# Kernel tuning notes

Hardware: AMD Instinct MI355X
Metric: run time of the kernel (lower is better)

## Reference

```python
import jax, jax.numpy as jnp
import numpy as np

H = 512
B = 64
S = 2048
NUM_LAYERS = 1


def setup_inputs() -> dict:
    key = jax.random.key(0)
    ks = jax.random.split(key, 8)
    scale = 1.0 / np.sqrt(H)
    return {
        "hidden": jax.random.normal(ks[0], (NUM_LAYERS, B, H), dtype=jnp.float32),
        "encoder_outputs": jax.random.normal(ks[1], (B, S, H), dtype=jnp.float32),
        "U_w": jax.random.uniform(ks[2], (H, H), jnp.float32, -scale, scale),
        "U_b": jax.random.uniform(ks[3], (H,), jnp.float32, -scale, scale),
        "W_w": jax.random.uniform(ks[4], (H, H), jnp.float32, -scale, scale),
        "W_b": jax.random.uniform(ks[5], (H,), jnp.float32, -scale, scale),
        "V_w": jax.random.uniform(ks[6], (1, H), jnp.float32, -scale, scale),
        "V_b": jax.random.uniform(ks[7], (1,), jnp.float32, -scale, scale),
    }


def reference(hidden, encoder_outputs, U_w, U_b, W_w, W_b, V_w, V_b):
    # hidden: [L, B, H] -> take last layer, like hidden[-1]
    h = hidden[-1]  # [B, H]
    # Uatt(h): [B, H] -> broadcast over src_len
    u = h @ U_w.T + U_b            # [B, H]
    w = jnp.einsum('bsh,kh->bsk', encoder_outputs, W_w) + W_b  # [B, S, H]
    combined = jnp.tanh(u[:, None, :] + w)                     # [B, S, H]
    energy = jnp.einsum('bsh,h->bs', combined, V_w[0]) + V_b[0]  # [B, S]
    attn = jax.nn.softmax(energy, axis=1)                       # [B, S]
    context = jnp.einsum('bs,bsh->bh', attn, encoder_outputs)   # [B, H]
    return (context, attn)
```

## Files before the change

### kernel.cpp

```cpp
#include <hip/hip_runtime.h>
#include <hip/hip_bf16.h>

#define H 512
#define B 64
#define S 2048

typedef __bf16 bf16x8 __attribute__((ext_vector_type(8)));
typedef float f32x4 __attribute__((ext_vector_type(4)));
typedef unsigned int u32x4 __attribute__((ext_vector_type(4)));

__device__ __forceinline__ unsigned cvt2(float x, float y) {
    union { __hip_bfloat162 h; unsigned u; } cv;
    cv.h = __float22bfloat162_rn(make_float2(x, y));
    return cv.u;
}

__device__ __forceinline__ float fast_tanh(float x) {
    float e = __expf(2.0f * x);
    float r = __builtin_amdgcn_rcpf(e + 1.0f);
    return 1.0f - 2.0f * r;
}

__device__ __forceinline__ void gload_lds16(const void* g, void* l) {
    __builtin_amdgcn_global_load_lds(
        (const __attribute__((address_space(1))) unsigned int*)g,
        (__attribute__((address_space(3))) unsigned int*)l, 16, 0, 0);
}

__global__ __launch_bounds__(256) void w16_kernel(const float* __restrict__ Ww,
                                                  unsigned short* __restrict__ w16) {
    const int i = (blockIdx.x * 256 + threadIdx.x) * 8;
    float4 a = *(const float4*)(Ww + i);
    float4 b = *(const float4*)(Ww + i + 4);
    uint4 p;
    p.x = cvt2(a.x, a.y); p.y = cvt2(a.z, a.w);
    p.z = cvt2(b.x, b.y); p.w = cvt2(b.z, b.w);
    *(uint4*)(w16 + i) = p;
}

__global__ __launch_bounds__(256) void u_kernel(
        const float* __restrict__ hid, const float* __restrict__ Uw,
        const float* __restrict__ Ub, const float* __restrict__ Wb,
        float* __restrict__ u) {
    const int b = blockIdx.y;
    const int k = blockIdx.x * 4 + (threadIdx.x >> 6);
    const int lane = threadIdx.x & 63;
    const float4* wrow = (const float4*)(Uw + (size_t)k * H);
    const float4* hrow = (const float4*)(hid + (size_t)b * H);
    float4 w0 = wrow[lane * 2], w1 = wrow[lane * 2 + 1];
    float4 h0 = hrow[lane * 2], h1 = hrow[lane * 2 + 1];
    float acc = w0.x * h0.x + w0.y * h0.y + w0.z * h0.z + w0.w * h0.w
              + w1.x * h1.x + w1.y * h1.y + w1.z * h1.z + w1.w * h1.w;
    #pragma unroll
    for (int off = 1; off < 64; off <<= 1) acc += __shfl_xor(acc, off, 64);
    if (lane == 0) u[b * H + k] = acc + Ub[k] + Wb[k];
}

#define CN  32
#define NCH 16
#define CHB (CN * H * 2)

__global__ __launch_bounds__(512, 4) void energy_kernel(
        const float* __restrict__ enc, const unsigned short* __restrict__ w16,
        const float* __restrict__ Vw, const float* __restrict__ u,
        float* __restrict__ energy) {
    const int s0  = blockIdx.x * 128;
    const int b   = blockIdx.y;
    const int tid = threadIdx.x;
    const int wave = tid >> 6, lane = tid & 63;
    const int quad = lane >> 4, c = lane & 15;

    __shared__ unsigned char Bs[2][CHB];
    __shared__ float uS[H], vS[H];

    #pragma unroll
    for (int i = 0; i < 4; ++i) {
        const int row = i * 8 + wave;
        const int d   = (row << 10) + lane * 16;
        gload_lds16((const unsigned char*)w16 + (d ^ ((row & 7) << 4)),
                    &Bs[0][row << 10]);
    }

    uS[tid] = u[b * H + tid];
    vS[tid] = Vw[tid];

    u32x4 apack[16];
    {
        const float* pa = enc + ((size_t)(b * S + s0 + wave * 16 + c)) * H + quad * 8;
        #pragma unroll
        for (int half = 0; half < 2; ++half) {
            float4 x0[8], x1[8];
            #pragma unroll
            for (int q = 0; q < 8; ++q) {
                const int t = half * 8 + q;
                x0[q] = *(const float4*)(pa + t * 32);
                x1[q] = *(const float4*)(pa + t * 32 + 4);
            }
            #pragma unroll
            for (int q = 0; q < 8; ++q) {
                u32x4 p;
                p[0] = cvt2(x0[q].x, x0[q].y); p[1] = cvt2(x0[q].z, x0[q].w);
                p[2] = cvt2(x1[q].x, x1[q].y); p[3] = cvt2(x1[q].z, x1[q].w);
                apack[half * 8 + q] = p;
                asm volatile("" : "+v"(apack[half * 8 + q]));
            }
        }
    }

    float esum[4] = {};
    const int mask = (c & 7) << 4;

    #pragma unroll 2
    for (int cc = 0; cc < NCH; ++cc) {
        const int buf = cc & 1;
        if (cc) __syncthreads();
        if (cc < NCH - 1) {
            const unsigned char* src = (const unsigned char*)w16 + (cc + 1) * CHB;
            #pragma unroll
            for (int i = 0; i < 4; ++i) {
                const int row = i * 8 + wave;
                const int d   = (row << 10) + lane * 16;
                gload_lds16(src + (d ^ ((row & 7) << 4)), &Bs[buf ^ 1][row << 10]);
            }
            asm volatile("s_waitcnt vmcnt(4)" ::: "memory");
        } else {
            asm volatile("s_waitcnt vmcnt(0)" ::: "memory");
        }
        __syncthreads();

        const unsigned char* bb = Bs[buf];
        f32x4 acc[2] = {};
        __builtin_amdgcn_s_setprio(1);
        #pragma unroll
        for (int t = 0; t < 16; ++t) {
            const int base = t * 64 + quad * 16;
            bf16x8 b0 = *(const bf16x8*)(bb + ((( c       << 10) + base) ^ mask));
            bf16x8 b1 = *(const bf16x8*)(bb + ((((16 + c) << 10) + base) ^ mask));
            acc[0] = __builtin_amdgcn_mfma_f32_16x16x32_bf16(*(const bf16x8*)&apack[t], b0, acc[0], 0, 0, 0);
            acc[1] = __builtin_amdgcn_mfma_f32_16x16x32_bf16(*(const bf16x8*)&apack[t], b1, acc[1], 0, 0, 0);
        }
        __builtin_amdgcn_s_setprio(0);
        #pragma unroll
        for (int ct = 0; ct < 2; ++ct) {
            const int col = cc * CN + ct * 16 + c;
            const float vv = vS[col], uu = uS[col];
            #pragma unroll
            for (int r = 0; r < 4; ++r)
                esum[r] += vv * fast_tanh(uu + acc[ct][r]);
        }
    }

    #pragma unroll
    for (int r = 0; r < 4; ++r) {
        float e = esum[r];
        e += __shfl_xor(e, 1, 64);
        e += __shfl_xor(e, 2, 64);
        e += __shfl_xor(e, 4, 64);
        e += __shfl_xor(e, 8, 64);
        if (c == 0)
            energy[b * S + s0 + wave * 16 + quad * 4 + r] = e;
    }
}

__global__ void softmax_kernel(const float* __restrict__ energy, float* __restrict__ attn) {
    int b = blockIdx.x;
    int t = threadIdx.x;
    const float* e = energy + b * S;
    float v[8];
    float m = -1e30f;
    #pragma unroll
    for (int i = 0; i < 8; ++i) { v[i] = e[t + i * 256]; m = fmaxf(m, v[i]); }
    #pragma unroll
    for (int off = 1; off < 64; off <<= 1) m = fmaxf(m, __shfl_xor(m, off, 64));
    __shared__ float redm[4], reds[4];
    if ((t & 63) == 0) redm[t >> 6] = m;
    __syncthreads();
    m = fmaxf(fmaxf(redm[0], redm[1]), fmaxf(redm[2], redm[3]));
    float s = 0.f;
    #pragma unroll
    for (int i = 0; i < 8; ++i) { v[i] = __expf(v[i] - m); s += v[i]; }
    #pragma unroll
    for (int off = 1; off < 64; off <<= 1) s += __shfl_xor(s, off, 64);
    if ((t & 63) == 0) reds[t >> 6] = s;
    __syncthreads();
    float inv = 1.0f / (reds[0] + reds[1] + reds[2] + reds[3]);
    #pragma unroll
    for (int i = 0; i < 8; ++i) attn[b * S + t + i * 256] = v[i] * inv;
}

#define CCH 128
__global__ __launch_bounds__(256) void context_kernel(
        const float* __restrict__ enc, const float* __restrict__ attn,
        float* __restrict__ ctx) {
    const int b  = blockIdx.x >> 4;
    const int ch = blockIdx.x & 15;
    const int t  = threadIdx.x;
    const int grp = t >> 7;
    const int ln  = t & 127;
    __shared__ float aS[CCH];
    __shared__ float red[H];
    if (t < CCH) aS[t] = attn[b * S + ch * CCH + t];
    __syncthreads();
    const float* ebase = enc + ((size_t)(b * S + ch * CCH) + grp * 64) * H + ln * 4;
    float4 acc = make_float4(0.f, 0.f, 0.f, 0.f);
    #pragma unroll 8
    for (int s = 0; s < 64; ++s) {
        const float a = aS[grp * 64 + s];
        const float4 e = *(const float4*)(ebase + (size_t)s * H);
        acc.x += a * e.x; acc.y += a * e.y; acc.z += a * e.z; acc.w += a * e.w;
    }
    if (grp == 0) *(float4*)&red[ln * 4] = acc;
    __syncthreads();
    if (grp == 1) {
        const float4 r = *(const float4*)&red[ln * 4];
        atomicAdd(&ctx[b * H + ln * 4 + 0], acc.x + r.x);
        atomicAdd(&ctx[b * H + ln * 4 + 1], acc.y + r.y);
        atomicAdd(&ctx[b * H + ln * 4 + 2], acc.z + r.z);
        atomicAdd(&ctx[b * H + ln * 4 + 3], acc.w + r.w);
    }
}

extern "C" void kernel_launch(void* const* d_in, const int* in_sizes, int n_in,
                              void* d_out, int out_size, void* d_ws, size_t ws_size,
                              hipStream_t stream) {
    (void)in_sizes; (void)n_in; (void)out_size; (void)ws_size;
    const float* hid = (const float*)d_in[0];
    const float* enc = (const float*)d_in[1];
    const float* Uw  = (const float*)d_in[2];
    const float* Ub  = (const float*)d_in[3];
    const float* Ww  = (const float*)d_in[4];
    const float* Wb  = (const float*)d_in[5];
    const float* Vw  = (const float*)d_in[6];

    float* out_ctx  = (float*)d_out;
    float* out_attn = out_ctx + B * H;
    float* energy   = (float*)d_ws;
    float* u        = energy + B * S;
    unsigned short* w16 = (unsigned short*)(u + B * H);

    hipMemsetAsync(d_out, 0, (size_t)B * H * sizeof(float), stream);

    w16_kernel<<<dim3(H * H / (256 * 8)), 256, 0, stream>>>(Ww, w16);
    u_kernel<<<dim3(H / 4, B), 256, 0, stream>>>(hid, Uw, Ub, Wb, u);
    energy_kernel<<<dim3(S / 128, B), 512, 0, stream>>>(enc, w16, Vw, u, energy);
    softmax_kernel<<<B, 256, 0, stream>>>(energy, out_attn);
    context_kernel<<<B * 16, 256, 0, stream>>>(enc, out_attn, out_ctx);
}
```

Measured before the change: 490.6 us.

## Restructure energy GEMM: stage encoder rows in LDS, stream W from global

The energy kernel now puts a 64-row bf16 tile of encoder outputs in swizzled shared memory, loaded in four pipelined K-phases. Each wave computes a 64x64 output tile with 4x4 MFMA accumulators, reading W fragments straight from global/L2 instead of double-buffering W chunks through LDS. Per-wave partial energies are reduced across waves via a shared-memory buffer. This raises MFMA reuse per fragment load and removes the W LDS pipeline, but it doubles the block count, uses 64KB+ of LDS per block (limiting occupancy), and depends on L2 for repeated W reads.

```diff
diff --git a/kernel.cpp b/kernel.cpp
--- a/kernel.cpp
+++ b/kernel.cpp
@@ -7,7 +7,6 @@
 
 typedef __bf16 bf16x8 __attribute__((ext_vector_type(8)));
 typedef float f32x4 __attribute__((ext_vector_type(4)));
-typedef unsigned int u32x4 __attribute__((ext_vector_type(4)));
 
 __device__ __forceinline__ unsigned cvt2(float x, float y) {
     union { __hip_bfloat162 h; unsigned u; } cv;
@@ -19,12 +18,6 @@
     float e = __expf(2.0f * x);
     float r = __builtin_amdgcn_rcpf(e + 1.0f);
     return 1.0f - 2.0f * r;
-}
-
-__device__ __forceinline__ void gload_lds16(const void* g, void* l) {
-    __builtin_amdgcn_global_load_lds(
-        (const __attribute__((address_space(1))) unsigned int*)g,
-        (__attribute__((address_space(3))) unsigned int*)l, 16, 0, 0);
 }
 
 __global__ __launch_bounds__(256) void w16_kernel(const float* __restrict__ Ww,
@@ -56,110 +49,113 @@
     if (lane == 0) u[b * H + k] = acc + Ub[k] + Wb[k];
 }
 
-#define CN  32
-#define NCH 16
-#define CHB (CN * H * 2)
-
 __global__ __launch_bounds__(512, 4) void energy_kernel(
         const float* __restrict__ enc, const unsigned short* __restrict__ w16,
         const float* __restrict__ Vw, const float* __restrict__ u,
         float* __restrict__ energy) {
-    const int s0  = blockIdx.x * 128;
+    const int s0  = blockIdx.x * 64;
     const int b   = blockIdx.y;
     const int tid = threadIdx.x;
     const int wave = tid >> 6, lane = tid & 63;
     const int quad = lane >> 4, c = lane & 15;
 
-    __shared__ unsigned char Bs[2][CHB];
+    __shared__ unsigned short As[64][512];
     __shared__ float uS[H], vS[H];
-
-    #pragma unroll
-    for (int i = 0; i < 4; ++i) {
-        const int row = i * 8 + wave;
-        const int d   = (row << 10) + lane * 16;
-        gload_lds16((const unsigned char*)w16 + (d ^ ((row & 7) << 4)),
-                    &Bs[0][row << 10]);
-    }
-
+    __shared__ float red[8][64];
+
+    const int arow = tid >> 3;
+    const int a8   = tid & 7;
+    const int akey = arow & 7;
+    const float* pa = enc + ((size_t)(b * S + s0 + arow)) * H + a8 * 16;
+    unsigned char* arowbase = (unsigned char*)&As[arow][0];
+
+    float4 av0, av1, av2, av3;
+#define ALOAD(p) { const float4* q_ = (const float4*)(pa + (p) * 128);         \
+    av0 = q_[0]; av1 = q_[1]; av2 = q_[2]; av3 = q_[3]; }
+#define AWRITE(p) { uint4 lo_, hi_;                                            \
+    lo_.x = cvt2(av0.x, av0.y); lo_.y = cvt2(av0.z, av0.w);                    \
+    lo_.z = cvt2(av1.x, av1.y); lo_.w = cvt2(av1.z, av1.w);                    \
+    hi_.x = cvt2(av2.x, av2.y); hi_.y = cvt2(av2.z, av2.w);                    \
+    hi_.z = cvt2(av3.x, av3.y); hi_.w = cvt2(av3.z, av3.w);                    \
+    const int ci_ = (p) * 16 + a8 * 2;                                         \
+    *(uint4*)(arowbase + (((ci_)     ^ akey) << 4)) = lo_;                     \
+    *(uint4*)(arowbase + (((ci_ + 1) ^ akey) << 4)) = hi_; }
+
+    ALOAD(0);
     uS[tid] = u[b * H + tid];
     vS[tid] = Vw[tid];
-
-    u32x4 apack[16];
-    {
-        const float* pa = enc + ((size_t)(b * S + s0 + wave * 16 + c)) * H + quad * 8;
-        #pragma unroll
-        for (int half = 0; half < 2; ++half) {
-            float4 x0[8], x1[8];
-            #pragma unroll
-            for (int q = 0; q < 8; ++q) {
-                const int t = half * 8 + q;
-                x0[q] = *(const float4*)(pa + t * 32);
-                x1[q] = *(const float4*)(pa + t * 32 + 4);
-            }
-            #pragma unroll
-            for (int q = 0; q < 8; ++q) {
-                u32x4 p;
-                p[0] = cvt2(x0[q].x, x0[q].y); p[1] = cvt2(x0[q].z, x0[q].w);
-                p[2] = cvt2(x1[q].x, x1[q].y); p[3] = cvt2(x1[q].z, x1[q].w);
-                apack[half * 8 + q] = p;
-                asm volatile("" : "+v"(apack[half * 8 + q]));
-            }
+    AWRITE(0);
+    __syncthreads();
+
+    const f32x4 fzero = {0.f, 0.f, 0.f, 0.f};
+    f32x4 acc[4][4];
+    #pragma unroll
+    for (int i = 0; i < 4; ++i)
+        #pragma unroll
+        for (int j = 0; j < 4; ++j) acc[i][j] = fzero;
+
+    const unsigned short* wbase = w16 + (size_t)(wave * 64 + c) * H + quad * 8;
+
+    #pragma unroll
+    for (int p = 0; p < 4; ++p) {
+        if (p < 3) ALOAD(p + 1);
+        #pragma unroll
+        for (int k2 = 0; k2 < 4; ++k2) {
+            const int kt = p * 4 + k2;
+            bf16x8 bf[4], af[4];
+            #pragma unroll
+            for (int j = 0; j < 4; ++j)
+                bf[j] = *(const bf16x8*)(wbase + (size_t)j * 16 * H + kt * 32);
+            #pragma unroll
+            for (int i = 0; i < 4; ++i)
+                af[i] = *(const bf16x8*)((const unsigned char*)&As[i * 16 + c][0]
+                        + ((((kt * 4 + quad) ^ (c & 7))) << 4));
+            __builtin_amdgcn_s_setprio(1);
+            #pragma unroll
+            for (int i = 0; i < 4; ++i)
+                #pragma unroll
+                for (int j = 0; j < 4; ++j)
+                    acc[i][j] = __builtin_amdgcn_mfma_f32_16x16x32_bf16(af[i], bf[j], acc[i][j], 0, 0, 0);
+            __builtin_amdgcn_s_setprio(0);
         }
-    }
-
-    float esum[4] = {};
-    const int mask = (c & 7) << 4;
-
-    #pragma unroll 2
-    for (int cc = 0; cc < NCH; ++cc) {
-        const int buf = cc & 1;
-        if (cc) __syncthreads();
-        if (cc < NCH - 1) {
-            const unsigned char* src = (const unsigned char*)w16 + (cc + 1) * CHB;
-            #pragma unroll
-            for (int i = 0; i < 4; ++i) {
-                const int row = i * 8 + wave;
-                const int d   = (row << 10) + lane * 16;
-                gload_lds16(src + (d ^ ((row & 7) << 4)), &Bs[buf ^ 1][row << 10]);
-            }
-            asm volatile("s_waitcnt vmcnt(4)" ::: "memory");
-        } else {
-            asm volatile("s_waitcnt vmcnt(0)" ::: "memory");
+        if (p < 3) { AWRITE(p + 1); __syncthreads(); }
+    }
+
+    float esum[4][4];
+    #pragma unroll
+    for (int i = 0; i < 4; ++i)
+        #pragma unroll
+        for (int r = 0; r < 4; ++r) esum[i][r] = 0.f;
+    #pragma unroll
+    for (int j = 0; j < 4; ++j) {
+        const int col = wave * 64 + j * 16 + c;
+        const float vv = vS[col], uu = uS[col];
+        #pragma unroll
+        for (int i = 0; i < 4; ++i)
+            #pragma unroll
+            for (int r = 0; r < 4; ++r)
+                esum[i][r] += vv * fast_tanh(uu + acc[i][j][r]);
+    }
+    #pragma unroll
+    for (int i = 0; i < 4; ++i)
+        #pragma unroll
+        for (int r = 0; r < 4; ++r) {
+            float e = esum[i][r];
+            e += __shfl_xor(e, 1, 64);
+            e += __shfl_xor(e, 2, 64);
+            e += __shfl_xor(e, 4, 64);
+            e += __shfl_xor(e, 8, 64);
+            if (c == 0) red[wave][i * 16 + quad * 4 + r] = e;
         }
-        __syncthreads();
-
-        const unsigned char* bb = Bs[buf];
-        f32x4 acc[2] = {};
-        __builtin_amdgcn_s_setprio(1);
-        #pragma unroll
-        for (int t = 0; t < 16; ++t) {
-            const int base = t * 64 + quad * 16;
-            bf16x8 b0 = *(const bf16x8*)(bb + ((( c       << 10) + base) ^ mask));
-            bf16x8 b1 = *(const bf16x8*)(bb + ((((16 + c) << 10) + base) ^ mask));
-            acc[0] = __builtin_amdgcn_mfma_f32_16x16x32_bf16(*(const bf16x8*)&apack[t], b0, acc[0], 0, 0, 0);
-            acc[1] = __builtin_amdgcn_mfma_f32_16x16x32_bf16(*(const bf16x8*)&apack[t], b1, acc[1], 0, 0, 0);
-        }
-        __builtin_amdgcn_s_setprio(0);
-        #pragma unroll
-        for (int ct = 0; ct < 2; ++ct) {
-            const int col = cc * CN + ct * 16 + c;
-            const float vv = vS[col], uu = uS[col];
-            #pragma unroll
-            for (int r = 0; r < 4; ++r)
-                esum[r] += vv * fast_tanh(uu + acc[ct][r]);
-        }
-    }
-
-    #pragma unroll
-    for (int r = 0; r < 4; ++r) {
-        float e = esum[r];
-        e += __shfl_xor(e, 1, 64);
-        e += __shfl_xor(e, 2, 64);
-        e += __shfl_xor(e, 4, 64);
-        e += __shfl_xor(e, 8, 64);
-        if (c == 0)
-            energy[b * S + s0 + wave * 16 + quad * 4 + r] = e;
-    }
+    __syncthreads();
+    if (tid < 64) {
+        float s = 0.f;
+        #pragma unroll
+        for (int w = 0; w < 8; ++w) s += red[w][tid];
+        energy[b * S + s0 + tid] = s;
+    }
+#undef ALOAD
+#undef AWRITE
 }
 
 __global__ void softmax_kernel(const float* __restrict__ energy, float* __restrict__ attn) {
@@ -242,7 +238,7 @@
 
     w16_kernel<<<dim3(H * H / (256 * 8)), 256, 0, stream>>>(Ww, w16);
     u_kernel<<<dim3(H / 4, B), 256, 0, stream>>>(hid, Uw, Ub, Wb, u);
-    energy_kernel<<<dim3(S / 128, B), 512, 0, stream>>>(enc, w16, Vw, u, energy);
+    energy_kernel<<<dim3(S / 64, B), 512, 0, stream>>>(enc, w16, Vw, u, energy);
     softmax_kernel<<<B, 256, 0, stream>>>(energy, out_attn);
     context_kernel<<<B * 16, 256, 0, stream>>>(enc, out_attn, out_ctx);
 }
```

After: 500.7 us. 1.02x slower.
